# Kernel optimization log

Measured on AMD Instinct MI355X. Metric: run time of the kernel, lower is better.

## Reference

```python
import jax, jax.numpy as jnp
import numpy as np

B, C, H, W = 32, 512, 64, 64
NBCLASS = 17


def setup_inputs() -> dict:
    key = jax.random.key(0)
    k1, k2 = jax.random.split(key, 2)
    x = jax.random.normal(k1, (B, C, H, W), dtype=jnp.float32)
    # 1x1 conv == linear over channels: weight (nbclass, C), bias (nbclass,)
    w_class = jax.random.normal(k2, (NBCLASS, C), dtype=jnp.float32) * 0.02
    b_class = jnp.zeros((NBCLASS,), dtype=jnp.float32)
    return {"x": x, "w_class": w_class, "b_class": b_class}


def reference(x, w_class, b_class):
    # x: (B, C, H, W); w_class: (K, C); b_class: (K,)
    Bx, Cx, Hx, Wx = x.shape
    # g = convclass(adaptive_avg_pool(x)) flattened -> (B, K)
    g = jnp.mean(x, axis=(2, 3)) @ w_class.T + b_class
    # cam = convclass(x) -> (B, K, H, W)
    cam = jnp.einsum('kc,bchw->bkhw', w_class, x) + b_class[None, :, None, None]
    # sf = mean_{h,w} sigmoid(cam)[:,k] * x[:,c]  -> (B, K, C)
    # (fused form of the original repeat/broadcast-multiply-mean)
    sf = jnp.einsum('bkhw,bchw->bkc', jax.nn.sigmoid(cam), x) / (Hx * Wx)
    return (g, sf)
```

## Files before the change

kernel.cpp:

```cpp
#include <hip/hip_runtime.h>
#include <cmath>

#define BATCH 32
#define CCH 512
#define HW 4096
#define KCL 17

typedef __attribute__((ext_vector_type(8))) short short8;
typedef __attribute__((ext_vector_type(16))) float f32x16;

__device__ __forceinline__ unsigned pack_bf16(float a, float b) {
  unsigned ua = (__float_as_uint(a) + 0x8000u) >> 16;
  unsigned ub = (__float_as_uint(b) + 0x8000u) & 0xFFFF0000u;
  return ua | ub;
}
__device__ __forceinline__ float bf_lo(unsigned u) { return __uint_as_float(u << 16); }
__device__ __forceinline__ float bf_hi(unsigned u) { return __uint_as_float(u & 0xFFFF0000u); }

#define WT_OFF 0
#define WT_BYTES (CCH * 20 * 4)
#define PART_OFF WT_BYTES
#define PART_BYTES (BATCH * 4 * KCL * HW * 2)
#define SIG_OFF (PART_OFF + PART_BYTES)
#define SIG_BYTES (BATCH * 32 * HW * 2)
#define WS_NEED (SIG_OFF + SIG_BYTES)

__global__ void transpose_w_kernel(const float* __restrict__ w, float* __restrict__ wT) {
  int c = threadIdx.x;
  #pragma unroll
  for (int k = 0; k < 20; ++k)
    wT[c * 20 + k] = (k < KCL) ? w[k * CCH + c] : 0.f;
}

__global__ __launch_bounds__(512)
void k1_campart(const float* __restrict__ x, const float* __restrict__ wT,
                unsigned short* __restrict__ part) {
  const int blk = blockIdx.x;
  const int b = blk >> 3;
  const int slab = (blk >> 1) & 3;
  const int pxq = blk & 1;
  const int px0 = pxq * 2048 + threadIdx.x * 4;
  const float* xp = x + (size_t)(b * CCH + slab * 128) * HW + px0;

  float cam[KCL][4];
  #pragma unroll
  for (int k = 0; k < KCL; ++k)
    #pragma unroll
    for (int i = 0; i < 4; ++i) cam[k][i] = 0.f;

  #pragma unroll 4
  for (int c = 0; c < 128; ++c) {
    const float4 v = *reinterpret_cast<const float4*>(xp + (size_t)c * HW);
    const float* wr = wT + (slab * 128 + c) * 20;
    #pragma unroll
    for (int k = 0; k < KCL; ++k) {
      cam[k][0] = fmaf(wr[k], v.x, cam[k][0]);
      cam[k][1] = fmaf(wr[k], v.y, cam[k][1]);
      cam[k][2] = fmaf(wr[k], v.z, cam[k][2]);
      cam[k][3] = fmaf(wr[k], v.w, cam[k][3]);
    }
  }

  unsigned short* pp = part + ((size_t)b * 4 + slab) * KCL * HW + px0;
  #pragma unroll
  for (int k = 0; k < KCL; ++k) {
    uint2 u = make_uint2(pack_bf16(cam[k][0], cam[k][1]), pack_bf16(cam[k][2], cam[k][3]));
    *reinterpret_cast<uint2*>(pp + (size_t)k * HW) = u;
  }
}

__global__ __launch_bounds__(512)
void k2_sig(const unsigned short* __restrict__ part, const float* __restrict__ bias,
            float* __restrict__ out_g, unsigned short* __restrict__ sig) {
  const int b = blockIdx.x / KCL;
  const int k = blockIdx.x - b * KCL;
  const int t = threadIdx.x;
  const float bk = bias[k];
  const int px0 = t * 8;
  const size_t SL = (size_t)KCL * HW;
  const unsigned short* pb = part + ((size_t)b * 4) * SL + (size_t)k * HW + px0;

  unsigned a0[4], a1[4], a2[4], a3[4];
  *reinterpret_cast<uint4*>(a0) = *reinterpret_cast<const uint4*>(pb);
  *reinterpret_cast<uint4*>(a1) = *reinterpret_cast<const uint4*>(pb + SL);
  *reinterpret_cast<uint4*>(a2) = *reinterpret_cast<const uint4*>(pb + 2 * SL);
  *reinterpret_cast<uint4*>(a3) = *reinterpret_cast<const uint4*>(pb + 3 * SL);

  float gs = 0.f;
  unsigned so[4];
  #pragma unroll
  for (int j = 0; j < 4; ++j) {
    float c0 = bk + bf_lo(a0[j]) + bf_lo(a1[j]) + bf_lo(a2[j]) + bf_lo(a3[j]);
    float c1 = bk + bf_hi(a0[j]) + bf_hi(a1[j]) + bf_hi(a2[j]) + bf_hi(a3[j]);
    gs += c0 + c1;
    float s0 = 1.f / (1.f + __expf(-c0));
    float s1 = 1.f / (1.f + __expf(-c1));
    so[j] = pack_bf16(s0, s1);
  }
  *reinterpret_cast<uint4*>(sig + ((size_t)b * 32 + k) * HW + px0) =
      *reinterpret_cast<uint4*>(so);

  const int lane = t & 63, wv = t >> 6;
  #pragma unroll
  for (int o = 1; o < 64; o <<= 1) gs += __shfl_xor(gs, o, 64);
  __shared__ float gr[8];
  if (lane == 0) gr[wv] = gs;
  __syncthreads();
  if (t == 0) {
    float s = gr[0] + gr[1] + gr[2] + gr[3] + gr[4] + gr[5] + gr[6] + gr[7];
    out_g[b * KCL + k] = s * (1.f / 4096.f);
  }
}

__global__ __launch_bounds__(512, 2)
void k3_sf(const float* __restrict__ x, const unsigned short* __restrict__ sig,
           float* __restrict__ out_sf) {
  extern __shared__ char smem[];
  const int t = threadIdx.x;
  const int lane = t & 63;
  const int wv = __builtin_amdgcn_readfirstlane(t >> 6);
  const int b = blockIdx.x >> 4;
  const int chs = blockIdx.x & 15;
  const float* xb = x + (size_t)(b * CCH + chs * 32) * HW;
  const int m = lane & 31;
  const int h = lane >> 5;
  const unsigned short* sigrow = sig + ((size_t)b * 32 + m) * HW;

  f32x16 acc;
  #pragma unroll
  for (int i = 0; i < 16; ++i) acc[i] = 0.f;

  #pragma unroll
  for (int j = 0; j < 16; ++j) {
    int mm = t + 512 * j;
    int row = mm >> 8;
    int q = mm & 255;
    const float4 v = *reinterpret_cast<const float4*>(xb + (size_t)row * HW + q * 4);
    unsigned u0 = pack_bf16(v.x, v.y);
    unsigned u1 = pack_bf16(v.z, v.w);
    *reinterpret_cast<uint2*>(smem + row * 2048 + ((q >> 1) ^ row) * 16 + (q & 1) * 8) =
        make_uint2(u0, u1);
  }
  __syncthreads();

  int cur = 0;
  float4 stg[16];
  for (int step = 0; step < 4; ++step) {
    if (step < 3) {
      #pragma unroll
      for (int j = 0; j < 16; ++j) {
        int mm = t + 512 * j;
        int row = mm >> 8;
        int q = mm & 255;
        stg[j] = *reinterpret_cast<const float4*>(
            xb + (size_t)row * HW + (step + 1) * 1024 + q * 4);
      }
    }
    const char* bufc = smem + cur * 65536;
    #pragma unroll
    for (int ks = 0; ks < 8; ++ks) {
      const int slin = wv * 16 + ks * 2 + h;
      const short8 a = *reinterpret_cast<const short8*>(bufc + m * 2048 + (slin ^ m) * 16);
      const short8 bb = *reinterpret_cast<const short8*>(
          sigrow + step * 1024 + wv * 128 + ks * 16 + h * 8);
      acc = __builtin_amdgcn_mfma_f32_32x32x16_bf16(a, bb, acc, 0, 0, 0);
    }
    if (step < 3) {
      char* bufn = smem + (cur ^ 1) * 65536;
      #pragma unroll
      for (int j = 0; j < 16; ++j) {
        int mm = t + 512 * j;
        int row = mm >> 8;
        int q = mm & 255;
        unsigned u0 = pack_bf16(stg[j].x, stg[j].y);
        unsigned u1 = pack_bf16(stg[j].z, stg[j].w);
        *reinterpret_cast<uint2*>(bufn + row * 2048 + ((q >> 1) ^ row) * 16 + (q & 1) * 8) =
            make_uint2(u0, u1);
      }
    }
    __syncthreads();
    cur ^= 1;
  }

  float* P = (float*)smem;
  #pragma unroll
  for (int r = 0; r < 16; ++r) {
    const int chr = (r & 3) + 8 * (r >> 2) + 4 * h;
    P[wv * 1024 + m * 32 + chr] = acc[r];
  }
  __syncthreads();
  const float inv = 1.f / 4096.f;
  {
    float s = 0.f;
    #pragma unroll
    for (int w8 = 0; w8 < 8; ++w8) s += P[w8 * 1024 + t];
    const int n = t >> 5, ch = t & 31;
    out_sf[((size_t)b * KCL + n) * CCH + chs * 32 + ch] = s * inv;
    if (t < 32) {
      float s2 = 0.f;
      #pragma unroll
      for (int w8 = 0; w8 < 8; ++w8) s2 += P[w8 * 1024 + 512 + t];
      out_sf[((size_t)b * KCL + 16) * CCH + chs * 32 + t] = s2 * inv;
    }
  }
}

extern "C" void kernel_launch(void* const* d_in, const int* in_sizes, int n_in,
                              void* d_out, int out_size, void* d_ws, size_t ws_size,
                              hipStream_t stream) {
  const float* x = (const float*)d_in[0];
  const float* w = (const float*)d_in[1];
  const float* bias = (const float*)d_in[2];
  float* out = (float*)d_out;
  float* outg = out;
  float* outsf = out + BATCH * KCL;

  char* ws = (char*)d_ws;
  float* wT = (float*)(ws + WT_OFF);
  unsigned short* part = (unsigned short*)(ws + PART_OFF);
  unsigned short* sig = (unsigned short*)(ws + SIG_OFF);

  transpose_w_kernel<<<1, 512, 0, stream>>>(w, wT);
  k1_campart<<<256, 512, 0, stream>>>(x, wT, part);
  k2_sig<<<BATCH * KCL, 512, 0, stream>>>(part, bias, outg, sig);
  hipFuncSetAttribute((const void*)k3_sf, hipFuncAttributeMaxDynamicSharedMemorySize, 131072);
  k3_sf<<<BATCH * 16, 512, 131072, stream>>>(x, sig, outsf);
}
```

Before: 128.0 us.

## Fuse cam partial reduction and sigmoid into one kernel, cache bf16 x for MFMA pass

The first kernel now reduces the four channel-slab partial cams in shared memory, applies bias and sigmoid, and accumulates g with atomics, so the separate partial-sum kernel and its bf16 partial buffer go away. It also writes a bf16 copy of x while streaming it, and the sf kernel reads that half-size copy straight from global memory into MFMA instead of converting fp32 x through double-buffered LDS. This trades an extra 128MB bf16 write for a halved second read of x, with a block-index swizzle added in k3. The atomics and zero-init make g depend on float atomic ordering.

```diff
diff --git a/kernel.cpp b/kernel.cpp
--- a/kernel.cpp
+++ b/kernel.cpp
@@ -14,33 +14,35 @@
   unsigned ub = (__float_as_uint(b) + 0x8000u) & 0xFFFF0000u;
   return ua | ub;
 }
-__device__ __forceinline__ float bf_lo(unsigned u) { return __uint_as_float(u << 16); }
-__device__ __forceinline__ float bf_hi(unsigned u) { return __uint_as_float(u & 0xFFFF0000u); }
 
 #define WT_OFF 0
 #define WT_BYTES (CCH * 20 * 4)
-#define PART_OFF WT_BYTES
-#define PART_BYTES (BATCH * 4 * KCL * HW * 2)
-#define SIG_OFF (PART_OFF + PART_BYTES)
-#define SIG_BYTES (BATCH * 32 * HW * 2)
+#define XBF_OFF WT_BYTES
+#define XBF_BYTES ((size_t)BATCH * CCH * HW * 2)
+#define SIG_OFF (XBF_OFF + XBF_BYTES)
+#define SIG_BYTES ((size_t)BATCH * 32 * HW * 2)
 #define WS_NEED (SIG_OFF + SIG_BYTES)
 
-__global__ void transpose_w_kernel(const float* __restrict__ w, float* __restrict__ wT) {
+__global__ void k0_setup(const float* __restrict__ w, float* __restrict__ wT,
+                         float* __restrict__ out_g) {
   int c = threadIdx.x;
   #pragma unroll
-  for (int k = 0; k < 20; ++k)
-    wT[c * 20 + k] = (k < KCL) ? w[k * CCH + c] : 0.f;
+  for (int k = 0; k < 20; ++k) wT[c * 20 + k] = (k < KCL) ? w[k * CCH + c] : 0.f;
+  out_g[c] = 0.f;
+  if (c < BATCH * KCL - 512) out_g[512 + c] = 0.f;
 }
 
 __global__ __launch_bounds__(512)
-void k1_campart(const float* __restrict__ x, const float* __restrict__ wT,
-                unsigned short* __restrict__ part) {
-  const int blk = blockIdx.x;
-  const int b = blk >> 3;
-  const int slab = (blk >> 1) & 3;
-  const int pxq = blk & 1;
-  const int px0 = pxq * 2048 + threadIdx.x * 4;
-  const float* xp = x + (size_t)(b * CCH + slab * 128) * HW + px0;
+void k1_cam_sig(const float* __restrict__ x, const float* __restrict__ wT,
+                const float* __restrict__ bias, float* __restrict__ out_g,
+                unsigned short* __restrict__ xbf, unsigned short* __restrict__ sig) {
+  extern __shared__ float R[];
+  const int t = threadIdx.x;
+  const int slab = t >> 7;
+  const int pxg = t & 127;
+  const int b = blockIdx.x >> 3;
+  const int px0 = (blockIdx.x & 7) * 512;
+  const int px = px0 + pxg * 4;
 
   float cam[KCL][4];
   #pragma unroll
@@ -48,10 +50,16 @@
     #pragma unroll
     for (int i = 0; i < 4; ++i) cam[k][i] = 0.f;
 
-  #pragma unroll 4
+  const float* xp = x + ((size_t)(b * CCH + slab * 128)) * HW + px;
+  unsigned short* xbp = xbf + ((size_t)(b * CCH + slab * 128)) * HW + px;
+  const float* wp = wT + slab * 128 * 20;
+
+  #pragma unroll 2
   for (int c = 0; c < 128; ++c) {
     const float4 v = *reinterpret_cast<const float4*>(xp + (size_t)c * HW);
-    const float* wr = wT + (slab * 128 + c) * 20;
+    *reinterpret_cast<uint2*>(xbp + (size_t)c * HW) =
+        make_uint2(pack_bf16(v.x, v.y), pack_bf16(v.z, v.w));
+    const float* wr = wp + c * 20;
     #pragma unroll
     for (int k = 0; k < KCL; ++k) {
       cam[k][0] = fmaf(wr[k], v.x, cam[k][0]);
@@ -61,128 +69,81 @@
     }
   }
 
-  unsigned short* pp = part + ((size_t)b * 4 + slab) * KCL * HW + px0;
-  #pragma unroll
-  for (int k = 0; k < KCL; ++k) {
-    uint2 u = make_uint2(pack_bf16(cam[k][0], cam[k][1]), pack_bf16(cam[k][2], cam[k][3]));
-    *reinterpret_cast<uint2*>(pp + (size_t)k * HW) = u;
+  if (slab >= 2) {
+    float* Rb = R + (slab - 2) * (KCL * 512);
+    #pragma unroll
+    for (int k = 0; k < KCL; ++k)
+      *reinterpret_cast<float4*>(Rb + k * 512 + pxg * 4) =
+          make_float4(cam[k][0], cam[k][1], cam[k][2], cam[k][3]);
   }
-}
-
-__global__ __launch_bounds__(512)
-void k2_sig(const unsigned short* __restrict__ part, const float* __restrict__ bias,
-            float* __restrict__ out_g, unsigned short* __restrict__ sig) {
-  const int b = blockIdx.x / KCL;
-  const int k = blockIdx.x - b * KCL;
-  const int t = threadIdx.x;
-  const float bk = bias[k];
-  const int px0 = t * 8;
-  const size_t SL = (size_t)KCL * HW;
-  const unsigned short* pb = part + ((size_t)b * 4) * SL + (size_t)k * HW + px0;
-
-  unsigned a0[4], a1[4], a2[4], a3[4];
-  *reinterpret_cast<uint4*>(a0) = *reinterpret_cast<const uint4*>(pb);
-  *reinterpret_cast<uint4*>(a1) = *reinterpret_cast<const uint4*>(pb + SL);
-  *reinterpret_cast<uint4*>(a2) = *reinterpret_cast<const uint4*>(pb + 2 * SL);
-  *reinterpret_cast<uint4*>(a3) = *reinterpret_cast<const uint4*>(pb + 3 * SL);
-
-  float gs = 0.f;
-  unsigned so[4];
-  #pragma unroll
-  for (int j = 0; j < 4; ++j) {
-    float c0 = bk + bf_lo(a0[j]) + bf_lo(a1[j]) + bf_lo(a2[j]) + bf_lo(a3[j]);
-    float c1 = bk + bf_hi(a0[j]) + bf_hi(a1[j]) + bf_hi(a2[j]) + bf_hi(a3[j]);
-    gs += c0 + c1;
-    float s0 = 1.f / (1.f + __expf(-c0));
-    float s1 = 1.f / (1.f + __expf(-c1));
-    so[j] = pack_bf16(s0, s1);
+  __syncthreads();
+  if (slab < 2) {
+    const float* Rb = R + slab * (KCL * 512);
+    #pragma unroll
+    for (int k = 0; k < KCL; ++k) {
+      const float4 r = *reinterpret_cast<const float4*>(Rb + k * 512 + pxg * 4);
+      cam[k][0] += r.x; cam[k][1] += r.y; cam[k][2] += r.z; cam[k][3] += r.w;
+    }
   }
-  *reinterpret_cast<uint4*>(sig + ((size_t)b * 32 + k) * HW + px0) =
-      *reinterpret_cast<uint4*>(so);
-
-  const int lane = t & 63, wv = t >> 6;
-  #pragma unroll
-  for (int o = 1; o < 64; o <<= 1) gs += __shfl_xor(gs, o, 64);
-  __shared__ float gr[8];
-  if (lane == 0) gr[wv] = gs;
   __syncthreads();
-  if (t == 0) {
-    float s = gr[0] + gr[1] + gr[2] + gr[3] + gr[4] + gr[5] + gr[6] + gr[7];
-    out_g[b * KCL + k] = s * (1.f / 4096.f);
+  if (slab == 1) {
+    #pragma unroll
+    for (int k = 0; k < KCL; ++k)
+      *reinterpret_cast<float4*>(R + k * 512 + pxg * 4) =
+          make_float4(cam[k][0], cam[k][1], cam[k][2], cam[k][3]);
+  }
+  __syncthreads();
+  if (slab == 0) {
+    const float inv = 1.f / 4096.f;
+    #pragma unroll
+    for (int k = 0; k < KCL; ++k) {
+      const float4 r = *reinterpret_cast<const float4*>(R + k * 512 + pxg * 4);
+      const float bk = bias[k];
+      float cf0 = cam[k][0] + r.x + bk;
+      float cf1 = cam[k][1] + r.y + bk;
+      float cf2 = cam[k][2] + r.z + bk;
+      float cf3 = cam[k][3] + r.w + bk;
+      float gk = cf0 + cf1 + cf2 + cf3;
+      unsigned u0 = pack_bf16(1.f / (1.f + __expf(-cf0)), 1.f / (1.f + __expf(-cf1)));
+      unsigned u1 = pack_bf16(1.f / (1.f + __expf(-cf2)), 1.f / (1.f + __expf(-cf3)));
+      *reinterpret_cast<uint2*>(sig + ((size_t)(b * 32 + k)) * HW + px) = make_uint2(u0, u1);
+      #pragma unroll
+      for (int o = 1; o < 64; o <<= 1) gk += __shfl_xor(gk, o, 64);
+      if ((t & 63) == 0) atomicAdd(out_g + b * KCL + k, gk * inv);
+    }
   }
 }
 
 __global__ __launch_bounds__(512, 2)
-void k3_sf(const float* __restrict__ x, const unsigned short* __restrict__ sig,
+void k3_sf(const unsigned short* __restrict__ xbf, const unsigned short* __restrict__ sig,
            float* __restrict__ out_sf) {
-  extern __shared__ char smem[];
+  __shared__ float P[8 * 1024];
+  const int p = blockIdx.x;
+  const int lid = (p & 7) * 64 + (p >> 3);
+  const int b = lid >> 4;
+  const int chs = lid & 15;
   const int t = threadIdx.x;
   const int lane = t & 63;
   const int wv = __builtin_amdgcn_readfirstlane(t >> 6);
-  const int b = blockIdx.x >> 4;
-  const int chs = blockIdx.x & 15;
-  const float* xb = x + (size_t)(b * CCH + chs * 32) * HW;
   const int m = lane & 31;
   const int h = lane >> 5;
-  const unsigned short* sigrow = sig + ((size_t)b * 32 + m) * HW;
+
+  const unsigned short* ap = xbf + ((size_t)(b * CCH + chs * 32 + m)) * HW;
+  const unsigned short* bp = sig + ((size_t)(b * 32 + m)) * HW;
 
   f32x16 acc;
   #pragma unroll
   for (int i = 0; i < 16; ++i) acc[i] = 0.f;
 
-  #pragma unroll
-  for (int j = 0; j < 16; ++j) {
-    int mm = t + 512 * j;
-    int row = mm >> 8;
-    int q = mm & 255;
-    const float4 v = *reinterpret_cast<const float4*>(xb + (size_t)row * HW + q * 4);
-    unsigned u0 = pack_bf16(v.x, v.y);
-    unsigned u1 = pack_bf16(v.z, v.w);
-    *reinterpret_cast<uint2*>(smem + row * 2048 + ((q >> 1) ^ row) * 16 + (q & 1) * 8) =
-        make_uint2(u0, u1);
-  }
-  __syncthreads();
-
-  int cur = 0;
-  float4 stg[16];
-  for (int step = 0; step < 4; ++step) {
-    if (step < 3) {
-      #pragma unroll
-      for (int j = 0; j < 16; ++j) {
-        int mm = t + 512 * j;
-        int row = mm >> 8;
-        int q = mm & 255;
-        stg[j] = *reinterpret_cast<const float4*>(
-            xb + (size_t)row * HW + (step + 1) * 1024 + q * 4);
-      }
-    }
-    const char* bufc = smem + cur * 65536;
-    #pragma unroll
-    for (int ks = 0; ks < 8; ++ks) {
-      const int slin = wv * 16 + ks * 2 + h;
-      const short8 a = *reinterpret_cast<const short8*>(bufc + m * 2048 + (slin ^ m) * 16);
-      const short8 bb = *reinterpret_cast<const short8*>(
-          sigrow + step * 1024 + wv * 128 + ks * 16 + h * 8);
-      acc = __builtin_amdgcn_mfma_f32_32x32x16_bf16(a, bb, acc, 0, 0, 0);
-    }
-    if (step < 3) {
-      char* bufn = smem + (cur ^ 1) * 65536;
-      #pragma unroll
-      for (int j = 0; j < 16; ++j) {
-        int mm = t + 512 * j;
-        int row = mm >> 8;
-        int q = mm & 255;
-        unsigned u0 = pack_bf16(stg[j].x, stg[j].y);
-        unsigned u1 = pack_bf16(stg[j].z, stg[j].w);
-        *reinterpret_cast<uint2*>(bufn + row * 2048 + ((q >> 1) ^ row) * 16 + (q & 1) * 8) =
-            make_uint2(u0, u1);
-      }
-    }
-    __syncthreads();
-    cur ^= 1;
+  const int obase = (wv * 64 + h) * 8;
+  #pragma unroll 4
+  for (int i = 0; i < 32; ++i) {
+    const int o = obase + i * 16;
+    const short8 a = *reinterpret_cast<const short8*>(ap + o);
+    const short8 bb = *reinterpret_cast<const short8*>(bp + o);
+    acc = __builtin_amdgcn_mfma_f32_32x32x16_bf16(a, bb, acc, 0, 0, 0);
   }
 
-  float* P = (float*)smem;
   #pragma unroll
   for (int r = 0; r < 16; ++r) {
     const int chr = (r & 3) + 8 * (r >> 2) + 4 * h;
@@ -217,12 +178,15 @@
 
   char* ws = (char*)d_ws;
   float* wT = (float*)(ws + WT_OFF);
-  unsigned short* part = (unsigned short*)(ws + PART_OFF);
+  unsigned short* xbf = (unsigned short*)(ws + XBF_OFF);
   unsigned short* sig = (unsigned short*)(ws + SIG_OFF);
 
-  transpose_w_kernel<<<1, 512, 0, stream>>>(w, wT);
-  k1_campart<<<256, 512, 0, stream>>>(x, wT, part);
-  k2_sig<<<BATCH * KCL, 512, 0, stream>>>(part, bias, outg, sig);
-  hipFuncSetAttribute((const void*)k3_sf, hipFuncAttributeMaxDynamicSharedMemorySize, 131072);
-  k3_sf<<<BATCH * 16, 512, 131072, stream>>>(x, sig, outsf);
+  k0_setup<<<1, 512, 0, stream>>>(w, wT, outg);
+
+  const int k1_lds = 2 * KCL * 512 * 4;
+  hipFuncSetAttribute((const void*)k1_cam_sig,
+                      hipFuncAttributeMaxDynamicSharedMemorySize, k1_lds);
+  k1_cam_sig<<<BATCH * 8, 512, k1_lds, stream>>>(x, wT, bias, outg, xbf, sig);
+
+  k3_sf<<<BATCH * 16, 512, 0, stream>>>(xbf, sig, outsf);
 }
```

After: 276.9 us. 2.16x slower.

## Emit bf16 copy of x in cam pass and read it directly in sf kernel

Applied to the files above, without the earlier changes.

The first kernel now writes a bf16 copy of x to workspace while it already streams x for the cam partials. The sf kernel then reads that bf16 copy straight from global memory into MFMA operands, with no LDS staging, double buffering or fp32-to-bf16 conversion. Its block index is also remapped to spread batches across blocks. This halves the bytes k3 reads for x but adds a 128MB write in k1, so whether the total traffic drops depends on L2/MALL behaviour. It also needs a larger workspace.

```diff
diff --git a/kernel.cpp b/kernel.cpp
--- a/kernel.cpp
+++ b/kernel.cpp
@@ -22,8 +22,10 @@
 #define PART_OFF WT_BYTES
 #define PART_BYTES (BATCH * 4 * KCL * HW * 2)
 #define SIG_OFF (PART_OFF + PART_BYTES)
-#define SIG_BYTES (BATCH * 32 * HW * 2)
-#define WS_NEED (SIG_OFF + SIG_BYTES)
+#define SIG_BYTES ((size_t)BATCH * 32 * HW * 2)
+#define XBF_OFF (SIG_OFF + SIG_BYTES)
+#define XBF_BYTES ((size_t)BATCH * CCH * HW * 2)
+#define WS_NEED (XBF_OFF + XBF_BYTES)
 
 __global__ void transpose_w_kernel(const float* __restrict__ w, float* __restrict__ wT) {
   int c = threadIdx.x;
@@ -34,13 +36,14 @@
 
 __global__ __launch_bounds__(512)
 void k1_campart(const float* __restrict__ x, const float* __restrict__ wT,
-                unsigned short* __restrict__ part) {
+                unsigned short* __restrict__ part, unsigned short* __restrict__ xbf) {
   const int blk = blockIdx.x;
   const int b = blk >> 3;
   const int slab = (blk >> 1) & 3;
   const int pxq = blk & 1;
   const int px0 = pxq * 2048 + threadIdx.x * 4;
   const float* xp = x + (size_t)(b * CCH + slab * 128) * HW + px0;
+  unsigned short* xbp = xbf + (size_t)(b * CCH + slab * 128) * HW + px0;
 
   float cam[KCL][4];
   #pragma unroll
@@ -51,6 +54,8 @@
   #pragma unroll 4
   for (int c = 0; c < 128; ++c) {
     const float4 v = *reinterpret_cast<const float4*>(xp + (size_t)c * HW);
+    *reinterpret_cast<uint2*>(xbp + (size_t)c * HW) =
+        make_uint2(pack_bf16(v.x, v.y), pack_bf16(v.z, v.w));
     const float* wr = wT + (slab * 128 + c) * 20;
     #pragma unroll
     for (int k = 0; k < KCL; ++k) {
@@ -113,76 +118,35 @@
 }
 
 __global__ __launch_bounds__(512, 2)
-void k3_sf(const float* __restrict__ x, const unsigned short* __restrict__ sig,
+void k3_sf(const unsigned short* __restrict__ xbf, const unsigned short* __restrict__ sig,
            float* __restrict__ out_sf) {
-  extern __shared__ char smem[];
+  __shared__ float P[8 * 1024];
+  const int p = blockIdx.x;
+  const int lid = (p & 7) * 64 + (p >> 3);
+  const int b = lid >> 4;
+  const int chs = lid & 15;
   const int t = threadIdx.x;
   const int lane = t & 63;
   const int wv = __builtin_amdgcn_readfirstlane(t >> 6);
-  const int b = blockIdx.x >> 4;
-  const int chs = blockIdx.x & 15;
-  const float* xb = x + (size_t)(b * CCH + chs * 32) * HW;
   const int m = lane & 31;
   const int h = lane >> 5;
-  const unsigned short* sigrow = sig + ((size_t)b * 32 + m) * HW;
+
+  const unsigned short* ap = xbf + ((size_t)(b * CCH + chs * 32 + m)) * HW;
+  const unsigned short* bp = sig + ((size_t)(b * 32 + m)) * HW;
 
   f32x16 acc;
   #pragma unroll
   for (int i = 0; i < 16; ++i) acc[i] = 0.f;
 
-  #pragma unroll
-  for (int j = 0; j < 16; ++j) {
-    int mm = t + 512 * j;
-    int row = mm >> 8;
-    int q = mm & 255;
-    const float4 v = *reinterpret_cast<const float4*>(xb + (size_t)row * HW + q * 4);
-    unsigned u0 = pack_bf16(v.x, v.y);
-    unsigned u1 = pack_bf16(v.z, v.w);
-    *reinterpret_cast<uint2*>(smem + row * 2048 + ((q >> 1) ^ row) * 16 + (q & 1) * 8) =
-        make_uint2(u0, u1);
-  }
-  __syncthreads();
-
-  int cur = 0;
-  float4 stg[16];
-  for (int step = 0; step < 4; ++step) {
-    if (step < 3) {
-      #pragma unroll
-      for (int j = 0; j < 16; ++j) {
-        int mm = t + 512 * j;
-        int row = mm >> 8;
-        int q = mm & 255;
-        stg[j] = *reinterpret_cast<const float4*>(
-            xb + (size_t)row * HW + (step + 1) * 1024 + q * 4);
-      }
-    }
-    const char* bufc = smem + cur * 65536;
-    #pragma unroll
-    for (int ks = 0; ks < 8; ++ks) {
-      const int slin = wv * 16 + ks * 2 + h;
-      const short8 a = *reinterpret_cast<const short8*>(bufc + m * 2048 + (slin ^ m) * 16);
-      const short8 bb = *reinterpret_cast<const short8*>(
-          sigrow + step * 1024 + wv * 128 + ks * 16 + h * 8);
-      acc = __builtin_amdgcn_mfma_f32_32x32x16_bf16(a, bb, acc, 0, 0, 0);
-    }
-    if (step < 3) {
-      char* bufn = smem + (cur ^ 1) * 65536;
-      #pragma unroll
-      for (int j = 0; j < 16; ++j) {
-        int mm = t + 512 * j;
-        int row = mm >> 8;
-        int q = mm & 255;
-        unsigned u0 = pack_bf16(stg[j].x, stg[j].y);
-        unsigned u1 = pack_bf16(stg[j].z, stg[j].w);
-        *reinterpret_cast<uint2*>(bufn + row * 2048 + ((q >> 1) ^ row) * 16 + (q & 1) * 8) =
-            make_uint2(u0, u1);
-      }
-    }
-    __syncthreads();
-    cur ^= 1;
+  const int obase = (wv * 64 + h) * 8;
+  #pragma unroll 4
+  for (int i = 0; i < 32; ++i) {
+    const int o = obase + i * 16;
+    const short8 a = *reinterpret_cast<const short8*>(ap + o);
+    const short8 bb = *reinterpret_cast<const short8*>(bp + o);
+    acc = __builtin_amdgcn_mfma_f32_32x32x16_bf16(a, bb, acc, 0, 0, 0);
   }
 
-  float* P = (float*)smem;
   #pragma unroll
   for (int r = 0; r < 16; ++r) {
     const int chr = (r & 3) + 8 * (r >> 2) + 4 * h;
@@ -219,10 +183,10 @@
   float* wT = (float*)(ws + WT_OFF);
   unsigned short* part = (unsigned short*)(ws + PART_OFF);
   unsigned short* sig = (unsigned short*)(ws + SIG_OFF);
+  unsigned short* xbf = (unsigned short*)(ws + XBF_OFF);
 
   transpose_w_kernel<<<1, 512, 0, stream>>>(w, wT);
-  k1_campart<<<256, 512, 0, stream>>>(x, wT, part);
+  k1_campart<<<256, 512, 0, stream>>>(x, wT, part, xbf);
   k2_sig<<<BATCH * KCL, 512, 0, stream>>>(part, bias, outg, sig);
-  hipFuncSetAttribute((const void*)k3_sf, hipFuncAttributeMaxDynamicSharedMemorySize, 131072);
-  k3_sf<<<BATCH * 16, 512, 131072, stream>>>(x, sig, outsf);
+  k3_sf<<<BATCH * 16, 512, 0, stream>>>(xbf, sig, outsf);
 }
```

After: 151.9 us. 18.6% more time.
